# Kernel tuning notes

Hardware: AMD Instinct MI355X
Metric: run time of the kernel (lower is better)

Reference implementation:

```python
import jax, jax.numpy as jnp
import numpy as np

B_GRAPHS = 256
N_PER = 512
N = B_GRAPHS * N_PER            # 131072 nodes
E = 1048576                     # edges (avg degree 8)
H = 64                          # hidden_dim
L = 3                           # num_layers
R = 128                         # rnn_dim
NODE_IN = 2
EDGE_IN = 2
OUT = 2
JK = L * H


def setup_inputs() -> dict:
    key = jax.random.key(0)
    ks = jax.random.split(key, 40)
    # intra-graph random edges
    g = jax.random.randint(ks[0], (E,), 0, B_GRAPHS)
    src = g * N_PER + jax.random.randint(ks[1], (E,), 0, N_PER)
    dst = g * N_PER + jax.random.randint(ks[2], (E,), 0, N_PER)
    edge_index = jnp.stack([src, dst]).astype(jnp.int64)
    batch = jnp.repeat(jnp.arange(B_GRAPHS, dtype=jnp.int64), N_PER)

    p = lambda k, shp: jax.random.normal(k, shp, jnp.float32) * 0.1
    return dict(
        x=jax.random.normal(ks[3], (N, NODE_IN), jnp.float32),
        edge_attr=jax.random.normal(ks[4], (E, EDGE_IN), jnp.float32),
        node_W=p(ks[5], (NODE_IN, H)), node_b=p(ks[6], (H,)),
        edgeemb_W=p(ks[7], (EDGE_IN, H)), edgeemb_b=p(ks[8], (H,)),
        gat_W=p(ks[9], (L, H, H)), gat_Wedge=p(ks[10], (L, H, H)),
        gat_att_src=p(ks[11], (L, H)), gat_att_dst=p(ks[12], (L, H)),
        gat_att_edge=p(ks[13], (L, H)), gat_b=p(ks[14], (L, H)),
        gru_wih_f=p(ks[15], (3 * R, JK)), gru_whh_f=p(ks[16], (3 * R, R)),
        gru_bih_f=p(ks[17], (3 * R,)), gru_bhh_f=p(ks[18], (3 * R,)),
        gru_wih_b=p(ks[19], (3 * R, JK)), gru_whh_b=p(ks[20], (3 * R, R)),
        gru_bih_b=p(ks[21], (3 * R,)), gru_bhh_b=p(ks[22], (3 * R,)),
        head_W1=p(ks[23], (2 * R, 64)), head_b1=p(ks[24], (64,)),
        head_W2=p(ks[25], (64, OUT)), head_b2=p(ks[26], (OUT,)),
        edge_index=edge_index, batch=batch,
    )


def _gru_dir(xs, wih, whh, bih, bhh):
    # xs: [T, B, F] -> outputs [T, B, R]  (PyTorch GRU cell equations)
    gx = xs @ wih.T + bih  # precompute input gates [T, B, 3R]
    h0 = jnp.zeros((xs.shape[1], R), xs.dtype)

    def step(h, g):
        gh = h @ whh.T + bhh
        r = jax.nn.sigmoid(g[..., :R] + gh[..., :R])
        z = jax.nn.sigmoid(g[..., R:2 * R] + gh[..., R:2 * R])
        n = jnp.tanh(g[..., 2 * R:] + r * gh[..., 2 * R:])
        hn = (1.0 - z) * n + z * h
        return hn, hn

    _, ys = jax.lax.scan(step, h0, gx)
    return ys


def _forward(x, edge_attr, node_W, node_b, edgeemb_W, edgeemb_b,
             gat_W, gat_Wedge, gat_att_src, gat_att_dst, gat_att_edge, gat_b,
             gru_wih_f, gru_whh_f, gru_bih_f, gru_bhh_f,
             gru_wih_b, gru_whh_b, gru_bih_b, gru_bhh_b,
             head_W1, head_b1, head_W2, head_b2, edge_index, batch):
    src, dst = edge_index[0], edge_index[1]
    h = x @ node_W + node_b                     # [N, H]
    e = edge_attr @ edgeemb_W + edgeemb_b       # [E, H]

    # PyG GATConv default add_self_loops=True, fill_value='mean':
    # self-loop edge feature = mean of incoming edge features per node
    ones = jnp.ones((E,), e.dtype)
    deg = jax.ops.segment_sum(ones, dst, num_segments=N)
    e_loop = jax.ops.segment_sum(e, dst, num_segments=N) / jnp.maximum(deg, 1.0)[:, None]
    ar = jnp.arange(N, dtype=src.dtype)
    srcF = jnp.concatenate([src, ar])
    dstF = jnp.concatenate([dst, ar])
    eF = jnp.concatenate([e, e_loop], axis=0)   # [E+N, H]

    outs = []
    for l in range(L):
        xp = h @ gat_W[l]                                   # [N, H]
        a_s = xp @ gat_att_src[l]                           # [N]
        a_d = xp @ gat_att_dst[l]                           # [N]
        a_e = (eF @ gat_Wedge[l]) @ gat_att_edge[l]         # [E+N]
        alpha = jax.nn.leaky_relu(a_s[srcF] + a_d[dstF] + a_e, 0.2)
        m = jax.ops.segment_max(alpha, dstF, num_segments=N)
        ex = jnp.exp(alpha - m[dstF])
        den = jax.ops.segment_sum(ex, dstF, num_segments=N)
        w = ex / den[dstF]                                  # segment softmax
        agg = jax.ops.segment_sum(w[:, None] * xp[srcF], dstF, num_segments=N) + gat_b[l]
        h = jax.nn.leaky_relu(agg, 0.01)                    # F.leaky_relu default slope
        outs.append(h)

    h_jk = jnp.concatenate(outs, axis=-1)                   # [N, JK]
    # to_dense_batch: sorted equal-size graphs -> dense reshape, mask all True
    dense = h_jk.reshape(B_GRAPHS, N_PER, JK)
    xs = dense.transpose(1, 0, 2)                           # [T, B, JK]
    yf = _gru_dir(xs, gru_wih_f, gru_whh_f, gru_bih_f, gru_bhh_f)
    yb = _gru_dir(xs[::-1], gru_wih_b, gru_whh_b, gru_bih_b, gru_bhh_b)[::-1]
    rnn_out = jnp.concatenate([yf, yb], axis=-1).transpose(1, 0, 2)  # [B, T, 2R]
    out = jax.nn.relu(rnn_out @ head_W1 + head_b1) @ head_W2 + head_b2
    return out.reshape(N, OUT)                              # out[mask], mask full


def reference(x, edge_attr, node_W, node_b, edgeemb_W, edgeemb_b,
              gat_W, gat_Wedge, gat_att_src, gat_att_dst, gat_att_edge, gat_b,
              gru_wih_f, gru_whh_f, gru_bih_f, gru_bhh_f,
              gru_wih_b, gru_whh_b, gru_bih_b, gru_bhh_b,
              head_W1, head_b1, head_W2, head_b2, edge_index, batch):
    return _forward(x, edge_attr, node_W, node_b, edgeemb_W, edgeemb_b,
                    gat_W, gat_Wedge, gat_att_src, gat_att_dst, gat_att_edge, gat_b,
                    gru_wih_f, gru_whh_f, gru_bih_f, gru_bhh_f,
                    gru_wih_b, gru_whh_b, gru_bih_b, gru_bhh_b,
                    head_W1, head_b1, head_W2, head_b2, edge_index, batch)
```

## Files before the change

kernel.cpp:

```cpp
#include <hip/hip_runtime.h>
#include <cstdint>
#include <cstddef>

typedef _Float16 half_t;
typedef _Float16 half8 __attribute__((ext_vector_type(8)));
typedef float f32x4 __attribute__((ext_vector_type(4)));

constexpr int NN = 131072;
constexpr int NE = 1048576;
constexpr int NPER = 512;

#define DEVINL __device__ __forceinline__

DEVINL float sigm_(float x){ float e = __expf(-x); return __builtin_amdgcn_rcpf(1.f+e); }
DEVINL float tanh_(float x){
  x = fminf(15.f, fmaxf(-15.f, x));
  float e = __expf(-2.f*x);
  return (1.f-e)*__builtin_amdgcn_rcpf(1.f+e);
}

#define LDS_BARRIER() asm volatile("s_waitcnt lgkmcnt(0)\ns_barrier" ::: "memory")

__global__ void prep_pack(const float* __restrict__ wih_f, const float* __restrict__ wih_b,
                          const float* __restrict__ head_W1, const float* __restrict__ gat_W,
                          const float* __restrict__ bih_f, const float* __restrict__ bih_b,
                          const float* __restrict__ bhh_f, const float* __restrict__ bhh_b,
                          const float* __restrict__ whh_f, const float* __restrict__ whh_b,
                          half_t* __restrict__ BcombT, half_t* __restrict__ W1T,
                          half_t* __restrict__ BTgat, float* __restrict__ bias_comb,
                          half_t* __restrict__ whh16,
                          const float* __restrict__ gatWe, const float* __restrict__ attE,
                          const float* __restrict__ eW, const float* __restrict__ eb,
                          float* __restrict__ cc){
  const int b = blockIdx.x;
  if (b >= 1075){
    int l = b - 1075, k = threadIdx.x;
    if (k < 64){
      const float* Wel = gatWe + l*4096;
      float s3=0.f;
      for (int j=0;j<64;j++) s3 += Wel[k*64+j]*attE[l*64+j];
      float c0 = eW[k]*s3, c1 = eW[64+k]*s3, cb = eb[k]*s3;
      for (int off=1; off<64; off<<=1){
        c0 += __shfl_xor(c0,off); c1 += __shfl_xor(c1,off); cb += __shfl_xor(cb,off);
      }
      if (k==0){ cc[l]=c0; cc[3+l]=c1; cc[6+l]=cb; }
    }
    return;
  }
  int gid = b*256 + threadIdx.x;
  if (gid < 147456){
    int j = gid/192, k = gid%192;
    float v = (j<384)? wih_f[j*192+k] : wih_b[(j-384)*192+k];
    BcombT[gid] = (half_t)v;
  } else if (gid < 163840){
    int i = gid - 147456;
    int n = i>>8, k = i&255;
    W1T[i] = (half_t)head_W1[k*64+n];
  } else if (gid < 176128){
    int i = gid - 163840;
    int l = i>>12, r = i&4095;
    int n = r>>6, k = r&63;
    BTgat[i] = (half_t)gat_W[l*4096 + k*64 + n];
  } else if (gid < 176896){
    int i = gid - 176128;
    float v;
    if (i < 256)       v = bih_f[i]     + bhh_f[i];
    else if (i < 384)  v = bih_f[i];
    else if (i < 640)  v = bih_b[i-384] + bhh_b[i-384];
    else               v = bih_b[i-384];
    bias_comb[i] = v;
  } else if (gid < 275200){
    int i = gid - 176896;
    float v = (i<49152)? whh_f[i] : whh_b[i-49152];
    whh16[i] = (half_t)v;
  }
}

__global__ __launch_bounds__(256) void embed_deg(const float* __restrict__ x,
                            const float* __restrict__ nW, const float* __restrict__ nb,
                            half_t* __restrict__ h,
                            const int* __restrict__ ei,
                            int* __restrict__ deg, int* __restrict__ tmp){
  const int b = blockIdx.x;
  if (b < 4096){
    int gid = b*256 + threadIdx.x;
    int n = gid>>3, j0 = (gid&7)*8;
    float x0 = x[2*n], x1 = x[2*n+1];
    half8 hv;
    #pragma unroll
    for (int u=0;u<8;u++){
      int j = j0+u;
      hv[u] = (half_t)(x0*nW[j] + x1*nW[64+j] + nb[j]);
    }
    *(half8*)(h + (size_t)n*64 + j0) = hv;
  } else {
    int e = (b-4096)*256 + threadIdx.x;
    int dt = ei[NE+e];
    tmp[e] = atomicAdd(&deg[dt],1);
  }
}

__global__ __launch_bounds__(256) void scan1(const int* __restrict__ deg, int* __restrict__ rowstart,
                      int* __restrict__ bsum){
  __shared__ int sc[256];
  int b=blockIdx.x, t=threadIdx.x, i=b*256+t;
  int v=deg[i]; sc[t]=v; __syncthreads();
  for (int off=1; off<256; off<<=1){
    int tv = (t>=off)? sc[t-off] : 0;
    __syncthreads(); sc[t]+=tv; __syncthreads();
  }
  rowstart[i]=sc[t]-v;
  if (t==255) bsum[b]=sc[255];
}
__global__ void scan2(int* __restrict__ bsum){
  __shared__ int sc[512];
  int t=threadIdx.x; int v=bsum[t]; sc[t]=v; __syncthreads();
  for (int off=1; off<512; off<<=1){
    int tv = (t>=off)? sc[t-off] : 0;
    __syncthreads(); sc[t]+=tv; __syncthreads();
  }
  bsum[t]=sc[t]-v;
}
__global__ __launch_bounds__(256) void scan3(int* __restrict__ rowstart, const int* __restrict__ bsum){
  int b=blockIdx.x, t=threadIdx.x, i=b*256+t;
  rowstart[i]+=bsum[b];
}

__global__ __launch_bounds__(256) void fill2(const int* __restrict__ ei, const float* __restrict__ ea,
                      const int* __restrict__ rowstart, const int* __restrict__ tmp,
                      int4* __restrict__ rec){
  int e = blockIdx.x*256 + threadIdx.x;
  int dt = ei[NE+e];
  int slot = rowstart[dt] + tmp[e];
  int4 r;
  r.x = ei[e];
  r.y = __float_as_int(ea[2*e]);
  r.z = __float_as_int(ea[2*e+1]);
  r.w = dt;
  rec[slot] = r;
}

__global__ __launch_bounds__(256) void gemm_xp(const half_t* __restrict__ A, int lda,
                        const half_t* __restrict__ BT,
                        const float* __restrict__ attS, const float* __restrict__ attD,
                        half_t* __restrict__ xp, float* __restrict__ a_s, float* __restrict__ a_d,
                        const int* __restrict__ deg, const int* __restrict__ rowstart,
                        const int4* __restrict__ rec, float2* __restrict__ m01){
  if (blockIdx.x >= 1024){
    int n = (blockIdx.x-1024)*256 + threadIdx.x;
    int st = rowstart[n], cnt = deg[n];
    float s0=0.f, s1=0.f;
    for (int i=0;i<cnt;i++){
      int4 r = rec[st+i];
      s0 += __int_as_float(r.y);
      s1 += __int_as_float(r.z);
    }
    float inv = 1.f/(float)max(cnt,1);
    float2 m; m.x = s0*inv; m.y = s1*inv;
    m01[n] = m;
    return;
  }
  __shared__ half_t As[128*32];
  __shared__ half_t Bs[64*32];
  const int tid = threadIdx.x, m0 = blockIdx.x*128;
  const int w = tid>>6, lane = tid&63;
  const int lm = lane&15, quad = lane>>4;
  const int wm0 = w*32;
  f32x4 acc[2][4] = {};
  for (int k0=0;k0<64;k0+=32){
    {
      const int c0 = tid*2;
      #pragma unroll
      for (int u=0;u<2;u++){
        int c=c0+u; int row=c>>2; int off=(c&3)*8;
        *(half8*)(&As[row*32+off]) = *(const half8*)(&A[(size_t)(m0+row)*lda + k0 + off]);
      }
      int c=tid; int row=c>>2; int off=(c&3)*8;
      *(half8*)(&Bs[row*32+off]) = *(const half8*)(&BT[(size_t)row*64 + k0 + off]);
    }
    __syncthreads();
    half8 af[2], bf[4];
    #pragma unroll
    for (int nt=0;nt<4;nt++) bf[nt] = *(const half8*)(&Bs[(nt*16+lm)*32 + quad*8]);
    #pragma unroll
    for (int mt=0;mt<2;mt++) af[mt] = *(const half8*)(&As[(wm0+mt*16+lm)*32 + quad*8]);
    #pragma unroll
    for (int mt=0;mt<2;mt++)
      #pragma unroll
      for (int nt=0;nt<4;nt++)
        acc[mt][nt] = __builtin_amdgcn_mfma_f32_16x16x32_f16(af[mt], bf[nt], acc[mt][nt], 0,0,0);
    __syncthreads();
  }
  float vsv[4], vdv[4];
  #pragma unroll
  for (int nt=0;nt<4;nt++){ vsv[nt]=attS[nt*16+lm]; vdv[nt]=attD[nt*16+lm]; }
  #pragma unroll
  for (int mt=0;mt<2;mt++)
   #pragma unroll
   for (int r=0;r<4;r++){
    int m = m0+wm0+mt*16+quad*4+r;
    float ps=0.f, pd=0.f;
    #pragma unroll
    for (int nt=0;nt<4;nt++){
      float v = acc[mt][nt][r];
      xp[(size_t)m*64 + nt*16+lm] = (half_t)v;
      ps += v*vsv[nt]; pd += v*vdv[nt];
    }
    ps += __shfl_xor(ps,1); ps += __shfl_xor(ps,2); ps += __shfl_xor(ps,4); ps += __shfl_xor(ps,8);
    pd += __shfl_xor(pd,1); pd += __shfl_xor(pd,2); pd += __shfl_xor(pd,4); pd += __shfl_xor(pd,8);
    if (lm==0){ a_s[m]=ps; a_d[m]=pd; }
  }
}

constexpr int SWCAP = 1536;
__global__ __launch_bounds__(512,4) void agg_lds(const int* __restrict__ rowstart, const int* __restrict__ deg,
                          const int4* __restrict__ rec,
                          const float* __restrict__ a_s, const float* __restrict__ a_d,
                          const float2* __restrict__ m01, const float* __restrict__ cc, int l,
                          const half_t* __restrict__ xp, const float* __restrict__ bias,
                          half_t* __restrict__ hjk){
  __shared__ int2  swl[SWCAP];
  __shared__ float nwsf[128];
  __shared__ int   ncnt[128];
  const int tid = threadIdx.x;
  const int nbase = blockIdx.x*128;
  const half_t* __restrict__ xpg = xp + ((size_t)(nbase >> 9))*32768;
  const int segst = rowstart[nbase];
  const int segend = rowstart[nbase+127] + deg[nbase+127];
  const int segcnt = segend - segst;
  const int w = tid>>6, lane = tid&63;
  const float c0 = cc[l], c1 = cc[3+l], cb = cc[6+l];
  int scap = segcnt < SWCAP ? segcnt : SWCAP;
  for (int i=tid; i<scap; i+=512){
    int4 r = rec[segst+i];
    float al = a_s[r.x] + a_d[r.w]
             + __int_as_float(r.y)*c0 + __int_as_float(r.z)*c1 + cb;
    al = al>0.f? al : 0.2f*al;
    int2 o;
    o.x = (r.x & 511) | ((r.w & 127) << 16);
    o.y = __float_as_int(__expf(al));
    swl[i] = o;
  }
  if (tid < 128){
    int n = nbase + tid;
    int cnt = deg[n];
    float2 m = m01[n];
    float ael = cnt? (m.x*c0 + m.y*c1 + cb) : 0.f;
    float asl = a_s[n] + a_d[n] + ael;
    asl = asl>0.f? asl : 0.2f*asl;
    nwsf[tid] = __expf(asl);
    ncnt[tid] = cnt;
  }
  const int e0 = rowstart[nbase + w*16] - segst;
  const int e1 = (w==7) ? segcnt : (rowstart[nbase + w*16 + 16] - segst);
  __syncthreads();
  const float bv = bias[lane];
  const int nlb = nbase & 511;

  auto flush = [&](int cur, float acc, float den){
    float wv = nwsf[cur];
    float xs = (float)xpg[(size_t)(nlb + cur)*64 + lane];
    float v = (acc + wv*xs)/(den + wv) + bv;
    v = v>0.f? v : 0.01f*v;
    hjk[(size_t)(nbase + cur)*192 + l*64 + lane] = (half_t)v;
  };

  if (segcnt <= SWCAP){
    const int cnt = e1 - e0;
    if (cnt > 0){
      int2  P[8];
      float X[8];
      #pragma unroll
      for (int i=0;i<8;i++){
        int idx = e0 + (i < cnt ? i : cnt-1);
        P[i] = swl[idx];
        X[i] = (float)xpg[(size_t)(P[i].x & 511)*64 + lane];
      }
      int cur = P[0].x >> 16;
      float acc = 0.f, den = 0.f;
      int e = e0;
      for (; e + 8 <= e1; e += 8){
        #pragma unroll
        for (int i=0;i<8;i++){
          int dl = P[i].x >> 16;
          if (dl != cur){ flush(cur, acc, den); cur = dl; acc = 0.f; den = 0.f; }
          float ww = __int_as_float(P[i].y);
          acc += ww*X[i]; den += ww;
          int nidx = e + 8 + i;
          int cidx = nidx < e1 ? nidx : e1-1;
          P[i] = swl[cidx];
          X[i] = (float)xpg[(size_t)(P[i].x & 511)*64 + lane];
        }
      }
      int rem = e1 - e;
      #pragma unroll
      for (int i=0;i<8;i++){
        if (i < rem){
          int dl = P[i].x >> 16;
          if (dl != cur){ flush(cur, acc, den); cur = dl; acc = 0.f; den = 0.f; }
          float ww = __int_as_float(P[i].y);
          acc += ww*X[i]; den += ww;
        }
      }
      flush(cur, acc, den);
    }
    #pragma unroll
    for (int i=0;i<16;i++){
      int li = w*16+i;
      if (ncnt[li]==0) flush(li, 0.f, 0.f);
    }
  } else {
    if (e0 < e1){
      auto mkw = [&](int idx)->int2{
        int4 r = rec[segst+idx];
        float al = a_s[r.x] + a_d[r.w]
                 + __int_as_float(r.y)*c0 + __int_as_float(r.z)*c1 + cb;
        al = al>0.f? al : 0.2f*al;
        int2 o;
        o.x = (r.x & 511) | ((r.w & 127) << 16);
        o.y = __float_as_int(__expf(al));
        return o;
      };
      int2 p = mkw(e0);
      float xv = (float)xpg[(size_t)(p.x & 511)*64 + lane];
      int cur = p.x >> 16;
      float acc = 0.f, den = 0.f;
      for (int e = e0; e < e1; ++e){
        int en = (e+1 < e1) ? e+1 : e;
        int2 pn = mkw(en);
        float xvn = (float)xpg[(size_t)(pn.x & 511)*64 + lane];
        int dl = p.x >> 16;
        if (dl != cur){
          flush(cur, acc, den);
          cur = dl; acc = 0.f; den = 0.f;
        }
        float ww = __int_as_float(p.y);
        acc += ww*xv; den += ww;
        p = pn; xv = xvn;
      }
      flush(cur, acc, den);
    }
    #pragma unroll
    for (int i=0;i<16;i++){
      int li = w*16+i;
      if (ncnt[li]==0) flush(li, 0.f, 0.f);
    }
  }
}

__global__ __launch_bounds__(256) void gemm_head(const half_t* __restrict__ A,
                        const half_t* __restrict__ W1T, const float* __restrict__ b1,
                        const float* __restrict__ W2, const float* __restrict__ b2,
                        float* __restrict__ out){
  __shared__ half_t As[128*32];
  __shared__ half_t Bs[64*32];
  const int tid = threadIdx.x, m0 = blockIdx.x*128;
  const int w = tid>>6, lane = tid&63;
  const int lm = lane&15, quad = lane>>4;
  const int wm0 = w*32;
  f32x4 acc[2][4] = {};
  for (int k0=0;k0<256;k0+=32){
    {
      const int c0 = tid*2;
      #pragma unroll
      for (int u=0;u<2;u++){
        int c=c0+u; int row=c>>2; int off=(c&3)*8;
        *(half8*)(&As[row*32+off]) = *(const half8*)(&A[(size_t)(m0+row)*256 + k0 + off]);
      }
      int c=tid; int row=c>>2; int off=(c&3)*8;
      *(half8*)(&Bs[row*32+off]) = *(const half8*)(&W1T[(size_t)row*256 + k0 + off]);
    }
    __syncthreads();
    half8 af[2], bf[4];
    #pragma unroll
    for (int nt=0;nt<4;nt++) bf[nt] = *(const half8*)(&Bs[(nt*16+lm)*32 + quad*8]);
    #pragma unroll
    for (int mt=0;mt<2;mt++) af[mt] = *(const half8*)(&As[(wm0+mt*16+lm)*32 + quad*8]);
    #pragma unroll
    for (int mt=0;mt<2;mt++)
      #pragma unroll
      for (int nt=0;nt<4;nt++)
        acc[mt][nt] = __builtin_amdgcn_mfma_f32_16x16x32_f16(af[mt], bf[nt], acc[mt][nt], 0,0,0);
    __syncthreads();
  }
  float b1v[4], w20[4], w21[4];
  #pragma unroll
  for (int nt=0;nt<4;nt++){
    int n = nt*16+lm;
    b1v[nt]=b1[n]; w20[nt]=W2[n*2]; w21[nt]=W2[n*2+1];
  }
  float b20=b2[0], b21=b2[1];
  #pragma unroll
  for (int mt=0;mt<2;mt++)
   #pragma unroll
   for (int r=0;r<4;r++){
    int m = m0+wm0+mt*16+quad*4+r;
    float p0=0.f, p1=0.f;
    #pragma unroll
    for (int nt=0;nt<4;nt++){
      float v = acc[mt][nt][r] + b1v[nt];
      v = v>0.f? v : 0.f;
      p0 += v*w20[nt]; p1 += v*w21[nt];
    }
    p0 += __shfl_xor(p0,1); p0 += __shfl_xor(p0,2); p0 += __shfl_xor(p0,4); p0 += __shfl_xor(p0,8);
    p1 += __shfl_xor(p1,1); p1 += __shfl_xor(p1,2); p1 += __shfl_xor(p1,4); p1 += __shfl_xor(p1,8);
    if (lm==0){
      out[(size_t)m*2]   = p0 + b20;
      out[(size_t)m*2+1] = p1 + b21;
    }
  }
}

__global__ __launch_bounds__(512,1) void gru_fused(
    const half_t* __restrict__ whh16, const float* __restrict__ bhh_f, const float* __restrict__ bhh_b,
    const half_t* __restrict__ gxf, const half_t* __restrict__ gxb,
    float* __restrict__ hstate, half_t* __restrict__ y, int c, int gruBlocks,
    const half_t* __restrict__ hjk, const half_t* __restrict__ BcombT, const float* __restrict__ biasc,
    half_t* __restrict__ gxf_n, half_t* __restrict__ gxb_n, int s0f, int s0b){
  __shared__ __align__(16) char SMEM[24832];
  const int bid = blockIdx.x;
  const int tid = threadIdx.x;
  if (bid < gruBlocks){
    __builtin_amdgcn_s_setprio(1);
    auto& H  = *(half_t (*)[2][16][132])SMEM;
    auto& YB = *(half_t (*)[16][4][128])(SMEM + 8448);
    const int d = bid >> 6, gblk = bid & 63;
    const half_t* __restrict__ gx = d ? gxb : gxf;
    const float* bhh = d ? bhh_b : bhh_f;
    const int w = tid >> 6, lane = tid & 63;
    const int l15 = lane & 15, quad = lane >> 4;
    const int unit = w*16 + l15;

    half8 bf[3][4];
    float bhn = bhh[256 + unit];
    {
      const half_t* wbase = whh16 + (size_t)d*49152;
      #pragma unroll
      for (int g=0; g<3; g++){
        const half_t* wp = wbase + (size_t)(g*128 + unit)*128;
        #pragma unroll
        for (int kk=0; kk<4; kk++)
          bf[g][kk] = *(const half8*)(wp + kk*32 + quad*8);
      }
    }

    float hreg = hstate[((size_t)d*256 + gblk*4 + quad)*128 + unit];

    const int jstep = d ? -384 : 384;
    const int j0 = d ? 127 : 0;
    const int pos0 = d ? (511 - c*128) : (c*128);

    const int dr  = tid >> 3;
    const int dg  = dr >> 4;
    const int dtl = dr & 15;
    const int dof = (tid & 7)*16;

    long gofs = ((long)(gblk*4 + quad)*128 + j0)*384 + unit;
    half_t A0,A1,A2, B0,B1,B2;
    A0 = gx[gofs]; A1 = gx[gofs+128]; A2 = gx[gofs+256]; gofs += jstep;
    B0 = gx[gofs]; B1 = gx[gofs+128]; B2 = gx[gofs+256]; gofs += jstep;

    H[0][quad*4][unit] = (half_t)hreg;
    LDS_BARRIER();

    auto stepf = [&](int t, int rd, int wr2, half_t& c0, half_t& c1, half_t& c2, bool pf){
      half8 af[4] = {};
      if ((l15 & 3) == 0){
        #pragma unroll
        for (int kk=0; kk<4; kk++)
          af[kk] = *(const half8*)&H[rd][l15][kk*32 + quad*8];
      }
      f32x4 Pa[3] = {}, Pb[3] = {};
      #pragma unroll
      for (int g=0; g<3; g++){
        Pa[g] = __builtin_amdgcn_mfma_f32_16x16x32_f16(af[0], bf[g][0], Pa[g], 0,0,0);
        Pb[g] = __builtin_amdgcn_mfma_f32_16x16x32_f16(af[2], bf[g][2], Pb[g], 0,0,0);
        Pa[g] = __builtin_amdgcn_mfma_f32_16x16x32_f16(af[1], bf[g][1], Pa[g], 0,0,0);
        Pb[g] = __builtin_amdgcn_mfma_f32_16x16x32_f16(af[3], bf[g][3], Pb[g], 0,0,0);
      }
      float p0 = Pa[0][0] + Pb[0][0];
      float p1 = Pa[1][0] + Pb[1][0];
      float p2 = Pa[2][0] + Pb[2][0];
      float rr = sigm_((float)c0 + p0);
      float zz = sigm_((float)c1 + p1);
      float nn = tanh_((float)c2 + rr*(p2 + bhn));
      float hn = nn + zz*(hreg - nn);
      hreg = hn;
      half_t hh = (half_t)hn;
      H[wr2][quad*4][unit] = hh;
      YB[t & 15][quad][unit] = hh;
      if (pf){
        c0 = gx[gofs]; c1 = gx[gofs+128]; c2 = gx[gofs+256];
        gofs += jstep;
      }
      LDS_BARRIER();
      if ((t & 15) == 15){
        int ts = (t - 15) + dtl;
        int pos = d ? (pos0 - ts) : (pos0 + ts);
        half_t* yp = y + ((size_t)(gblk*4 + dg)*512 + pos)*256 + d*128 + dof;
        uint4 v0 = *(const uint4*)&YB[dtl][dg][dof];
        uint4 v1 = *(const uint4*)&YB[dtl][dg][dof + 8];
        *(uint4*)yp = v0;
        *(uint4*)(yp + 8) = v1;
        LDS_BARRIER();
      }
    };

    for (int t=0; t<128; t+=2){
      stepf(t,   0, 1, A0,A1,A2, t < 126);
      stepf(t+1, 1, 0, B0,B1,B2, t < 126);
    }
    __builtin_amdgcn_s_setprio(0);
    hstate[((size_t)d*256 + gblk*4 + quad)*128 + unit] = hreg;
  } else {
    half_t* As = (half_t*)SMEM;
    half_t* Bs = (half_t*)(SMEM + 8192);
    const int gb = bid - gruBlocks;
    const int bx = gb & 255, by = gb >> 8;
    const int m0 = bx*128;
    const bool back = by >= 3;
    const int n0 = (back ? by-3 : by)*128;
    const int step0 = back ? s0b : s0f;
    half_t* C = back ? gxb_n : gxf_n;
    const half_t* BTh = BcombT + (back ? (size_t)384*192 : 0);
    const float* bh = biasc + (back ? 384 : 0);
    const int w = tid>>6, lane = tid&63;
    const int lm = lane&15, quad = lane>>4;
    const int wm0 = (w>>2)*64, wn0 = (w&3)*32;
    f32x4 acc[4][2] = {};
    for (int k0=0; k0<192; k0+=32){
      {
        int cidx = tid; int row = cidx>>2; int off = (cidx&3)*8;
        int m = m0+row;
        size_t arow = (size_t)(m>>7)*512 + step0 + (m&127);
        *(half8*)(&As[row*32+off]) = *(const half8*)(&hjk[arow*192 + k0 + off]);
        *(half8*)(&Bs[row*32+off]) = *(const half8*)(&BTh[(size_t)(n0+row)*192 + k0 + off]);
      }
      __syncthreads();
      half8 af[4], bfr[2];
      #pragma unroll
      for (int nt=0;nt<2;nt++) bfr[nt] = *(const half8*)(&Bs[(wn0+nt*16+lm)*32 + quad*8]);
      #pragma unroll
      for (int mt=0;mt<4;mt++) af[mt] = *(const half8*)(&As[(wm0+mt*16+lm)*32 + quad*8]);
      #pragma unroll
      for (int mt=0;mt<4;mt++)
        #pragma unroll
        for (int nt=0;nt<2;nt++)
          acc[mt][nt] = __builtin_amdgcn_mfma_f32_16x16x32_f16(af[mt], bfr[nt], acc[mt][nt], 0,0,0);
      __syncthreads();
    }
    #pragma unroll
    for (int mt=0;mt<4;mt++)
     #pragma unroll
     for (int nt=0;nt<2;nt++)
      #pragma unroll
      for (int r=0;r<4;r++){
        int m = m0+wm0+mt*16+quad*4+r;
        int n = n0+wn0+nt*16+lm;
        float v = acc[mt][nt][r] + bh[n];
        C[(size_t)m*384 + n] = (half_t)v;
      }
  }
}

extern "C" void kernel_launch(void* const* d_in, const int* in_sizes, int n_in,
                              void* d_out, int out_size, void* d_ws, size_t ws_size,
                              hipStream_t stream) {
  const float* x       = (const float*)d_in[0];
  const float* ea      = (const float*)d_in[1];
  const float* node_W  = (const float*)d_in[2];
  const float* node_b  = (const float*)d_in[3];
  const float* eW      = (const float*)d_in[4];
  const float* eb      = (const float*)d_in[5];
  const float* gat_W   = (const float*)d_in[6];
  const float* gat_We  = (const float*)d_in[7];
  const float* attS    = (const float*)d_in[8];
  const float* attD    = (const float*)d_in[9];
  const float* attE    = (const float*)d_in[10];
  const float* gat_b   = (const float*)d_in[11];
  const float* wih_f   = (const float*)d_in[12];
  const float* whh_f   = (const float*)d_in[13];
  const float* bih_f   = (const float*)d_in[14];
  const float* bhh_f   = (const float*)d_in[15];
  const float* wih_b   = (const float*)d_in[16];
  const float* whh_b   = (const float*)d_in[17];
  const float* bih_b   = (const float*)d_in[18];
  const float* bhh_b   = (const float*)d_in[19];
  const float* head_W1 = (const float*)d_in[20];
  const float* head_b1 = (const float*)d_in[21];
  const float* head_W2 = (const float*)d_in[22];
  const float* head_b2 = (const float*)d_in[23];
  const int*   ei      = (const int*)d_in[24];
  float* out = (float*)d_out;
  char* ws = (char*)d_ws;
  (void)in_sizes; (void)n_in; (void)out_size; (void)ws_size;

  size_t o = 0;
  auto alloc = [&](size_t bytes)->size_t{ size_t r=o; o += (bytes+255)&~(size_t)255; return r; };
  size_t o_cc     = alloc(16*4);
  size_t o_biasc  = alloc(768*4);
  size_t o_BcombT = alloc((size_t)768*192*2);
  size_t o_BTgat  = alloc((size_t)3*4096*2);
  size_t o_W1T    = alloc((size_t)64*256*2);
  size_t o_whh16  = alloc((size_t)2*49152*2);
  size_t o_hstate = alloc((size_t)2*256*128*4);
  size_t shared_base = o;

  size_t o_deg    = alloc((size_t)NN*4);
  size_t zero_end = o;
  size_t o_tmp    = alloc((size_t)NE*4);
  size_t o_rows   = alloc((size_t)NN*4);
  size_t o_bsum   = alloc(512*4);
  size_t o_rec    = alloc((size_t)NE*16);
  size_t o_m01    = alloc((size_t)NN*8);
  size_t o_as     = alloc((size_t)NN*4);
  size_t o_ad     = alloc((size_t)NN*4);
  size_t o_h      = alloc((size_t)NN*64*2);
  size_t o_xp     = alloc((size_t)NN*64*2);
  size_t gat_end  = o;
  size_t gat_size = gat_end - shared_base;

  const size_t GXC    = (size_t)256*128*384*2;
  const size_t HJK_SZ = (size_t)NN*192*2;
  size_t shared_sz = gat_size > 4*GXC ? gat_size : 4*GXC;
  size_t o_gx0f = shared_base;
  size_t o_gx0b = shared_base + GXC;
  size_t o_gx1f = shared_base + 2*GXC;
  size_t o_gx1b = shared_base + 3*GXC;
  size_t o_hjk = shared_base + shared_sz;
  size_t o_y   = o_hjk + HJK_SZ;

  int*    deg    = (int*)(ws+o_deg);
  int*    tmp    = (int*)(ws+o_tmp);
  int*    rows   = (int*)(ws+o_rows);
  int*    bsum   = (int*)(ws+o_bsum);
  int4*   rec    = (int4*)(ws+o_rec);
  float2* m01    = (float2*)(ws+o_m01);
  float*  a_s    = (float*)(ws+o_as);
  float*  a_d    = (float*)(ws+o_ad);
  float*  cc     = (float*)(ws+o_cc);
  float*  biasc  = (float*)(ws+o_biasc);
  half_t* h      = (half_t*)(ws+o_h);
  half_t* xp     = (half_t*)(ws+o_xp);
  half_t* hjk    = (half_t*)(ws+o_hjk);
  half_t* BcombT = (half_t*)(ws+o_BcombT);
  half_t* BTgat  = (half_t*)(ws+o_BTgat);
  half_t* W1T    = (half_t*)(ws+o_W1T);
  half_t* whh16  = (half_t*)(ws+o_whh16);
  float*  hstate = (float*)(ws+o_hstate);
  half_t* gxbuf[2][2] = {{(half_t*)(ws+o_gx0f), (half_t*)(ws+o_gx0b)},
                         {(half_t*)(ws+o_gx1f), (half_t*)(ws+o_gx1b)}};
  half_t* y      = (half_t*)(ws+o_y);

  hipMemsetAsync(ws+shared_base, 0, zero_end-shared_base, stream);
  hipMemsetAsync(ws+o_hstate, 0, (size_t)2*256*128*4, stream);

  prep_pack<<<1078,256,0,stream>>>(wih_f, wih_b, head_W1, gat_W, bih_f, bih_b, bhh_f, bhh_b,
                                   whh_f, whh_b,
                                   BcombT, W1T, BTgat, biasc, whh16,
                                   gat_We, attE, eW, eb, cc);
  embed_deg<<<8192,256,0,stream>>>(x, node_W, node_b, h, ei, deg, tmp);
  scan1<<<512,256,0,stream>>>(deg, rows, bsum);
  scan2<<<1,512,0,stream>>>(bsum);
  scan3<<<512,256,0,stream>>>(rows, bsum);
  fill2<<<4096,256,0,stream>>>(ei, ea, rows, tmp, rec);

  for (int l=0;l<3;l++){
    const half_t* in = (l==0)? h : (hjk + (size_t)(l-1)*64);
    int lda = (l==0)? 64 : 192;
    int grid = (l==0)? 1536 : 1024;
    gemm_xp<<<grid,256,0,stream>>>(in, lda, BTgat + (size_t)l*4096, attS + l*64, attD + l*64,
                                   xp, a_s, a_d, deg, rows, rec, m01);
    agg_lds<<<1024,512,0,stream>>>(rows, deg, rec, a_s, a_d, m01, cc, l, xp, gat_b + l*64, hjk);
  }

  gru_fused<<<1536,512,0,stream>>>(whh16, bhh_f, bhh_b, gxbuf[0][0], gxbuf[0][1], hstate, y, 0, 0,
                                   hjk, BcombT, biasc, gxbuf[0][0], gxbuf[0][1], 0, 384);
  for (int c=0;c<4;c++){
    int buf = c&1, nbuf = (c+1)&1;
    int grid = 128 + (c<3 ? 1536 : 0);
    gru_fused<<<grid,512,0,stream>>>(whh16, bhh_f, bhh_b, gxbuf[buf][0], gxbuf[buf][1], hstate, y, c, 128,
                                     hjk, BcombT, biasc, gxbuf[nbuf][0], gxbuf[nbuf][1],
                                     (c+1)*128, (2-c)*128);
  }

  gemm_head<<<1024,256,0,stream>>>(y, W1T, head_b1, head_W2, head_b2, out);
}
```

Measured before the change: 663.4 us.

## Overlap half of head GEMM with final GRU chunk and fuse scan3 into fill

The final GRU chunk launch now carries extra blocks that run the head MLP on the middle two 128-row tiles of each graph. Both GRU directions have already finished those time steps, so that work can overlap the latency-bound recurrence on otherwise idle CUs. A standalone gemm_head then handles only the first and last tiles. Separately, scan3 and fill2 are merged into one launch that writes offsets to a new rows2 buffer and adds the block sums inline while filling. The trade-off is that the extra head blocks compete with the GRU blocks for CUs and bandwidth, and the new offsets array costs a small amount of memory.

```diff
diff --git a/kernel.cpp b/kernel.cpp
--- a/kernel.cpp
+++ b/kernel.cpp
@@ -121,23 +121,26 @@
   }
   bsum[t]=sc[t]-v;
 }
-__global__ __launch_bounds__(256) void scan3(int* __restrict__ rowstart, const int* __restrict__ bsum){
-  int b=blockIdx.x, t=threadIdx.x, i=b*256+t;
-  rowstart[i]+=bsum[b];
-}
-
-__global__ __launch_bounds__(256) void fill2(const int* __restrict__ ei, const float* __restrict__ ea,
-                      const int* __restrict__ rowstart, const int* __restrict__ tmp,
-                      int4* __restrict__ rec){
-  int e = blockIdx.x*256 + threadIdx.x;
-  int dt = ei[NE+e];
-  int slot = rowstart[dt] + tmp[e];
-  int4 r;
-  r.x = ei[e];
-  r.y = __float_as_int(ea[2*e]);
-  r.z = __float_as_int(ea[2*e+1]);
-  r.w = dt;
-  rec[slot] = r;
+
+__global__ __launch_bounds__(256) void scan3_fill(const int* __restrict__ rowstart,
+                      const int* __restrict__ bsum, int* __restrict__ rows2,
+                      const int* __restrict__ ei, const float* __restrict__ ea,
+                      const int* __restrict__ tmp, int4* __restrict__ rec){
+  const int b = blockIdx.x;
+  if (b < 512){
+    int i = b*256 + threadIdx.x;
+    rows2[i] = rowstart[i] + bsum[b];
+  } else {
+    int e = (b-512)*256 + threadIdx.x;
+    int dt = ei[NE+e];
+    int slot = rowstart[dt] + bsum[dt>>8] + tmp[e];
+    int4 r;
+    r.x = ei[e];
+    r.y = __float_as_int(ea[2*e]);
+    r.z = __float_as_int(ea[2*e+1]);
+    r.w = dt;
+    rec[slot] = r;
+  }
 }
 
 __global__ __launch_bounds__(256) void gemm_xp(const half_t* __restrict__ A, int lda,
@@ -351,10 +354,11 @@
 __global__ __launch_bounds__(256) void gemm_head(const half_t* __restrict__ A,
                         const half_t* __restrict__ W1T, const float* __restrict__ b1,
                         const float* __restrict__ W2, const float* __restrict__ b2,
-                        float* __restrict__ out){
+                        float* __restrict__ out, int mode){
   __shared__ half_t As[128*32];
   __shared__ half_t Bs[64*32];
-  const int tid = threadIdx.x, m0 = blockIdx.x*128;
+  const int ib = mode ? ((blockIdx.x>>1)*4 + (blockIdx.x&1)*3) : blockIdx.x;
+  const int tid = threadIdx.x, m0 = ib*128;
   const int w = tid>>6, lane = tid&63;
   const int lm = lane&15, quad = lane>>4;
   const int wm0 = w*32;
@@ -414,9 +418,11 @@
 __global__ __launch_bounds__(512,1) void gru_fused(
     const half_t* __restrict__ whh16, const float* __restrict__ bhh_f, const float* __restrict__ bhh_b,
     const half_t* __restrict__ gxf, const half_t* __restrict__ gxb,
-    float* __restrict__ hstate, half_t* __restrict__ y, int c, int gruBlocks,
+    float* __restrict__ hstate, half_t* __restrict__ y, int c, int gruBlocks, int gxBlocks,
     const half_t* __restrict__ hjk, const half_t* __restrict__ BcombT, const float* __restrict__ biasc,
-    half_t* __restrict__ gxf_n, half_t* __restrict__ gxb_n, int s0f, int s0b){
+    half_t* __restrict__ gxf_n, half_t* __restrict__ gxb_n, int s0f, int s0b,
+    const half_t* __restrict__ W1T, const float* __restrict__ hb1,
+    const float* __restrict__ hW2, const float* __restrict__ hb2, float* __restrict__ out){
   __shared__ __align__(16) char SMEM[24832];
   const int bid = blockIdx.x;
   const int tid = threadIdx.x;
@@ -512,7 +518,7 @@
     }
     __builtin_amdgcn_s_setprio(0);
     hstate[((size_t)d*256 + gblk*4 + quad)*128 + unit] = hreg;
-  } else {
+  } else if (bid < gruBlocks + gxBlocks){
     half_t* As = (half_t*)SMEM;
     half_t* Bs = (half_t*)(SMEM + 8192);
     const int gb = bid - gruBlocks;
@@ -560,6 +566,71 @@
         float v = acc[mt][nt][r] + bh[n];
         C[(size_t)m*384 + n] = (half_t)v;
       }
+  } else {
+    half_t* As = (half_t*)SMEM;
+    half_t* Bs = (half_t*)(SMEM + 8192);
+    const int hb = bid - gruBlocks - gxBlocks;
+    const int ib = (hb>>1)*4 + 1 + (hb&1);
+    const int m0 = ib*128;
+    const bool act = tid < 256;
+    const int w = tid>>6, lane = tid&63;
+    const int lm = lane&15, quad = lane>>4;
+    const int wm0 = w*32;
+    f32x4 acc[2][4] = {};
+    for (int k0=0;k0<256;k0+=32){
+      if (act){
+        const int c0i = tid*2;
+        #pragma unroll
+        for (int u=0;u<2;u++){
+          int cx=c0i+u; int row=cx>>2; int off=(cx&3)*8;
+          *(half8*)(&As[row*32+off]) = *(const half8*)(&y[(size_t)(m0+row)*256 + k0 + off]);
+        }
+        int cx=tid; int row=cx>>2; int off=(cx&3)*8;
+        *(half8*)(&Bs[row*32+off]) = *(const half8*)(&W1T[(size_t)row*256 + k0 + off]);
+      }
+      __syncthreads();
+      if (act){
+        half8 af[2], bf[4];
+        #pragma unroll
+        for (int nt=0;nt<4;nt++) bf[nt] = *(const half8*)(&Bs[(nt*16+lm)*32 + quad*8]);
+        #pragma unroll
+        for (int mt=0;mt<2;mt++) af[mt] = *(const half8*)(&As[(wm0+mt*16+lm)*32 + quad*8]);
+        #pragma unroll
+        for (int mt=0;mt<2;mt++)
+          #pragma unroll
+          for (int nt=0;nt<4;nt++)
+            acc[mt][nt] = __builtin_amdgcn_mfma_f32_16x16x32_f16(af[mt], bf[nt], acc[mt][nt], 0,0,0);
+      }
+      __syncthreads();
+    }
+    if (act){
+      float b1v[4], w20[4], w21[4];
+      #pragma unroll
+      for (int nt=0;nt<4;nt++){
+        int n = nt*16+lm;
+        b1v[nt]=hb1[n]; w20[nt]=hW2[n*2]; w21[nt]=hW2[n*2+1];
+      }
+      float b20=hb2[0], b21=hb2[1];
+      #pragma unroll
+      for (int mt=0;mt<2;mt++)
+       #pragma unroll
+       for (int r=0;r<4;r++){
+        int m = m0+wm0+mt*16+quad*4+r;
+        float p0=0.f, p1=0.f;
+        #pragma unroll
+        for (int nt=0;nt<4;nt++){
+          float v = acc[mt][nt][r] + b1v[nt];
+          v = v>0.f? v : 0.f;
+          p0 += v*w20[nt]; p1 += v*w21[nt];
+        }
+        p0 += __shfl_xor(p0,1); p0 += __shfl_xor(p0,2); p0 += __shfl_xor(p0,4); p0 += __shfl_xor(p0,8);
+        p1 += __shfl_xor(p1,1); p1 += __shfl_xor(p1,2); p1 += __shfl_xor(p1,4); p1 += __shfl_xor(p1,8);
+        if (lm==0){
+          out[(size_t)m*2]   = p0 + b20;
+          out[(size_t)m*2+1] = p1 + b21;
+        }
+      }
+    }
   }
 }
 
@@ -610,6 +681,7 @@
   size_t zero_end = o;
   size_t o_tmp    = alloc((size_t)NE*4);
   size_t o_rows   = alloc((size_t)NN*4);
+  size_t o_rows2  = alloc((size_t)NN*4);
   size_t o_bsum   = alloc(512*4);
   size_t o_rec    = alloc((size_t)NE*16);
   size_t o_m01    = alloc((size_t)NN*8);
@@ -633,6 +705,7 @@
   int*    deg    = (int*)(ws+o_deg);
   int*    tmp    = (int*)(ws+o_tmp);
   int*    rows   = (int*)(ws+o_rows);
+  int*    rows2  = (int*)(ws+o_rows2);
   int*    bsum   = (int*)(ws+o_bsum);
   int4*   rec    = (int4*)(ws+o_rec);
   float2* m01    = (float2*)(ws+o_m01);
@@ -662,27 +735,29 @@
   embed_deg<<<8192,256,0,stream>>>(x, node_W, node_b, h, ei, deg, tmp);
   scan1<<<512,256,0,stream>>>(deg, rows, bsum);
   scan2<<<1,512,0,stream>>>(bsum);
-  scan3<<<512,256,0,stream>>>(rows, bsum);
-  fill2<<<4096,256,0,stream>>>(ei, ea, rows, tmp, rec);
+  scan3_fill<<<4608,256,0,stream>>>(rows, bsum, rows2, ei, ea, tmp, rec);
 
   for (int l=0;l<3;l++){
     const half_t* in = (l==0)? h : (hjk + (size_t)(l-1)*64);
     int lda = (l==0)? 64 : 192;
     int grid = (l==0)? 1536 : 1024;
     gemm_xp<<<grid,256,0,stream>>>(in, lda, BTgat + (size_t)l*4096, attS + l*64, attD + l*64,
-                                   xp, a_s, a_d, deg, rows, rec, m01);
-    agg_lds<<<1024,512,0,stream>>>(rows, deg, rec, a_s, a_d, m01, cc, l, xp, gat_b + l*64, hjk);
-  }
-
-  gru_fused<<<1536,512,0,stream>>>(whh16, bhh_f, bhh_b, gxbuf[0][0], gxbuf[0][1], hstate, y, 0, 0,
-                                   hjk, BcombT, biasc, gxbuf[0][0], gxbuf[0][1], 0, 384);
+                                   xp, a_s, a_d, deg, rows2, rec, m01);
+    agg_lds<<<1024,512,0,stream>>>(rows2, deg, rec, a_s, a_d, m01, cc, l, xp, gat_b + l*64, hjk);
+  }
+
+  gru_fused<<<1536,512,0,stream>>>(whh16, bhh_f, bhh_b, gxbuf[0][0], gxbuf[0][1], hstate, y, 0, 0, 1536,
+                                   hjk, BcombT, biasc, gxbuf[0][0], gxbuf[0][1], 0, 384,
+                                   W1T, head_b1, head_W2, head_b2, out);
   for (int c=0;c<4;c++){
     int buf = c&1, nbuf = (c+1)&1;
-    int grid = 128 + (c<3 ? 1536 : 0);
-    gru_fused<<<grid,512,0,stream>>>(whh16, bhh_f, bhh_b, gxbuf[buf][0], gxbuf[buf][1], hstate, y, c, 128,
+    int gxB = (c<3) ? 1536 : 0;
+    int grid = 128 + gxB + (c==3 ? 512 : 0);
+    gru_fused<<<grid,512,0,stream>>>(whh16, bhh_f, bhh_b, gxbuf[buf][0], gxbuf[buf][1], hstate, y, c, 128, gxB,
                                      hjk, BcombT, biasc, gxbuf[nbuf][0], gxbuf[nbuf][1],
-                                     (c+1)*128, (2-c)*128);
-  }
-
-  gemm_head<<<1024,256,0,stream>>>(y, W1T, head_b1, head_W2, head_b2, out);
-}
+                                     (c+1)*128, (2-c)*128,
+                                     W1T, head_b1, head_W2, head_b2, out);
+  }
+
+  gemm_head<<<512,256,0,stream>>>(y, W1T, head_b1, head_W2, head_b2, out, 1);
+}
```

New measurement: 659.6 us, median of 2. Within noise of the previous version (-0.6%).
